# Performance work log

Measured on AMD Instinct MI355X. Metric: run time of the kernel, lower is better.

The kernel has to match this reference:

```python
import jax, jax.numpy as jnp
import numpy as np

LOG2PI = float(np.log(2.0 * np.pi))
BN_EPS = 1e-5


def _spn_layer(x, scopes, mean, std, sum_w, bn_w, bn_b):
    """Vectorized SPNLayer of SPNNeurons.
    x:      [B, F]
    scopes: [O, F] int, per-neuron permutation of feature indices
    mean/std: [O, F//2, n_mv, 2] gaussian leaf params (pairs of features)
    sum_w:  [O, F//2, n_mv] sum-node mixture weights (softmax-normalized)
    bn_w, bn_b: [O] batchnorm affine params (training-mode batch stats)
    returns [B, O]
    """
    B = x.shape[0]
    O, P, M, _ = mean.shape
    # gather permuted features and group into pairs: [B, O, P, 2]
    xp = x[:, scopes].reshape(B, O, P, 2)
    # gaussian leaf log-likelihoods: [B, O, P, M, 2]
    z = (xp[:, :, :, None, :] - mean) / std
    ll = -0.5 * (z * z) - jnp.log(std) - 0.5 * LOG2PI
    # product node over each pair: [B, O, P, M]
    prod = ll.sum(axis=-1)
    # sum node: weighted mixture in log domain: [B, O, P]
    logw = jax.nn.log_softmax(sum_w, axis=-1)
    s = jax.nn.logsumexp(prod + logw, axis=-1)
    # root product node over all pairs: [B, O]
    out = s.sum(axis=-1)
    # BatchNorm1d (training mode, biased variance)
    mu = out.mean(axis=0)
    var = ((out - mu) ** 2).mean(axis=0)
    return (out - mu) / jnp.sqrt(var + BN_EPS) * bn_w + bn_b


def setup_inputs() -> dict:
    key = jax.random.key(0)
    ks = jax.random.split(key, 12)
    B, F_IN = 32768, 784
    H1, O1, O2, OUT = 32, 16, 10, 10
    n_mv = 2

    rng = np.random.RandomState(0)
    scopes1 = jnp.asarray(np.stack([rng.permutation(H1) for _ in range(O1)]), dtype=jnp.int32)
    scopes2 = jnp.asarray(np.stack([rng.permutation(O1) for _ in range(O2)]), dtype=jnp.int32)

    x = jax.random.normal(ks[0], (B, F_IN), jnp.float32)
    W1 = jax.random.normal(ks[1], (H1, F_IN), jnp.float32) * np.sqrt(2.0 / F_IN)
    b1 = jnp.zeros((H1,), jnp.float32)

    mean1 = jax.random.normal(ks[2], (O1, H1 // 2, n_mv, 2), jnp.float32)
    std1 = jax.random.uniform(ks[3], (O1, H1 // 2, n_mv, 2), jnp.float32, 0.5, 1.5)
    sw1 = jax.random.uniform(ks[4], (O1, H1 // 2, n_mv), jnp.float32)
    bn1_w = jnp.ones((O1,), jnp.float32)
    bn1_b = jnp.zeros((O1,), jnp.float32)

    mean2 = jax.random.normal(ks[5], (O2, O1 // 2, n_mv, 2), jnp.float32)
    std2 = jax.random.uniform(ks[6], (O2, O1 // 2, n_mv, 2), jnp.float32, 0.5, 1.5)
    sw2 = jax.random.uniform(ks[7], (O2, O1 // 2, n_mv), jnp.float32)
    bn2_w = jnp.ones((O2,), jnp.float32)
    bn2_b = jnp.zeros((O2,), jnp.float32)

    W2 = jax.random.normal(ks[8], (OUT, O2), jnp.float32) * np.sqrt(2.0 / O2)
    b2 = jnp.zeros((OUT,), jnp.float32)

    return {"x": x, "W1": W1, "b1": b1,
            "mean1": mean1, "std1": std1, "sw1": sw1, "bn1_w": bn1_w, "bn1_b": bn1_b,
            "mean2": mean2, "std2": std2, "sw2": sw2, "bn2_w": bn2_w, "bn2_b": bn2_b,
            "W2": W2, "b2": b2, "scopes1": scopes1, "scopes2": scopes2}


def reference(x, W1, b1, mean1, std1, sw1, bn1_w, bn1_b,
              mean2, std2, sw2, bn2_w, bn2_b, W2, b2, scopes1, scopes2):
    h = jax.nn.relu(x @ W1.T + b1)                                  # [B, 32]
    h = _spn_layer(h, scopes1, mean1, std1, sw1, bn1_w, bn1_b)      # [B, 16]
    h = _spn_layer(h, scopes2, mean2, std2, sw2, bn2_w, bn2_b)      # [B, 10]
    logits = h @ W2.T + b2                                          # [B, 10]
    return jax.nn.log_softmax(logits, axis=1)
```

## Files before the change

### kernel.cpp

```cpp
#include <hip/hip_runtime.h>
#include <hip/hip_bf16.h>
#include <math.h>

#define LOG2PI_F 1.8378770664093453f
#define BN_EPS 1e-5f
#define BATCH 32768

#define K1_ROWS 64
#define NB1 (BATCH / K1_ROWS)
#define WS1 840
#define NB3 1024
#define RPB3 32

typedef __attribute__((ext_vector_type(8))) short bf16x8;
typedef __attribute__((ext_vector_type(4))) float f32x4;

__global__ __launch_bounds__(256) void k0_cvt(
    const float* __restrict__ W1, __hip_bfloat16* __restrict__ w1h,
    __hip_bfloat16* __restrict__ w1l)
{
    int i = blockIdx.x * 256 + threadIdx.x;
    if (i >= 32 * WS1) return;
    int o = i / WS1, k = i - o * WS1;
    float w = (k < 784) ? W1[o * 784 + k] : 0.f;
    __hip_bfloat16 h = __float2bfloat16(w);
    float hf = __bfloat162float(h);
    __hip_bfloat16 l = __float2bfloat16(w - hf);
    w1h[i] = h;
    w1l[i] = l;
}

__global__ __launch_bounds__(256, 2) void k1_gemm_spn1(
    const float* __restrict__ x,
    const __hip_bfloat16* __restrict__ w1h, const __hip_bfloat16* __restrict__ w1l,
    const float* __restrict__ b1,
    const float* __restrict__ mean1, const float* __restrict__ std1, const float* __restrict__ sw1,
    const int* __restrict__ scopes1,
    float* __restrict__ s1, float* __restrict__ partials1)
{
    __shared__ __hip_bfloat16 Ah[64][72];
    __shared__ __hip_bfloat16 Al[64][72];
    __shared__ float h_lds[64][33];
    __shared__ float mu_l[1024], inv_l[1024], c0_l[512];
    __shared__ int   sc_l[512];
    __shared__ float b1_l[32];
    __shared__ float sv_l[16][66];

    const int t = threadIdx.x;

    for (int il = t; il < 1024; il += 256) {
        int o = il & 15, rest = il >> 4;
        int f = rest & 1, m = (rest >> 1) & 1, p = rest >> 2;
        int ig = ((o * 16 + p) * 2 + m) * 2 + f;
        mu_l[il]  = mean1[ig];
        inv_l[il] = 1.0f / std1[ig];
    }
    for (int il = t; il < 512; il += 256) {
        int o = il & 15, rest = il >> 4;
        int m = rest & 1, p = rest >> 1;
        int igw = (o * 16 + p) * 2;
        float w0 = sw1[igw], w1v = sw1[igw + 1];
        float mx = fmaxf(w0, w1v);
        float lse = mx + __logf(__expf(w0 - mx) + __expf(w1v - mx));
        float wm = (m == 0) ? w0 : w1v;
        int igs = ((o * 16 + p) * 2 + m) * 2;
        c0_l[il] = (wm - lse) - __logf(std1[igs]) - __logf(std1[igs + 1]) - LOG2PI_F;
    }
    for (int il = t; il < 512; il += 256) sc_l[il] = scopes1[il];
    if (t < 32) b1_l[t] = b1[t];

    const int wid  = t >> 6;
    const int lane = t & 63;
    const int row0 = blockIdx.x * K1_ROWS;

    f32x4 acc0 = {0.f, 0.f, 0.f, 0.f};
    f32x4 acc1 = {0.f, 0.f, 0.f, 0.f};

    float4 xr[4];
    #pragma unroll
    for (int i = 0; i < 4; ++i) {
        int idx = i * 256 + t;
        int rr = idx >> 4, kq = idx & 15;
        xr[i] = *(const float4*)(x + (size_t)(row0 + rr) * 784 + kq * 4);
    }

    for (int c = 0; c < 13; ++c) {
        __syncthreads();
        #pragma unroll
        for (int i = 0; i < 4; ++i) {
            int idx = i * 256 + t;
            int rr = idx >> 4, kq = idx & 15;
            float4 v = xr[i];
            float vv[4] = {v.x, v.y, v.z, v.w};
            #pragma unroll
            for (int e = 0; e < 4; ++e) {
                __hip_bfloat16 h = __float2bfloat16(vv[e]);
                float hf = __bfloat162float(h);
                Ah[rr][kq * 4 + e] = h;
                Al[rr][kq * 4 + e] = __float2bfloat16(vv[e] - hf);
            }
        }
        __syncthreads();
        if (c < 12) {
            int kbase = (c + 1) * 64;
            #pragma unroll
            for (int i = 0; i < 4; ++i) {
                int idx = i * 256 + t;
                int rr = idx >> 4, kq = idx & 15;
                int kg = kbase + kq * 4;
                if (kg < 784)
                    xr[i] = *(const float4*)(x + (size_t)(row0 + rr) * 784 + kg);
                else
                    xr[i] = make_float4(0.f, 0.f, 0.f, 0.f);
            }
        }
        int nsteps = (c == 12) ? 1 : 2;
        for (int s = 0; s < nsteps; ++s) {
            int kloc = s * 32 + ((lane >> 4) & 3) * 8;
            int arow = wid * 16 + (lane & 15);
            bf16x8 ah = *(const bf16x8*)(&Ah[arow][kloc]);
            bf16x8 al = *(const bf16x8*)(&Al[arow][kloc]);
            int kb = c * 64 + kloc;
            int o0 = lane & 15;
            bf16x8 wh0 = *(const bf16x8*)(&w1h[o0 * WS1 + kb]);
            bf16x8 wl0 = *(const bf16x8*)(&w1l[o0 * WS1 + kb]);
            bf16x8 wh1 = *(const bf16x8*)(&w1h[(16 + o0) * WS1 + kb]);
            bf16x8 wl1 = *(const bf16x8*)(&w1l[(16 + o0) * WS1 + kb]);
            acc0 = __builtin_amdgcn_mfma_f32_16x16x32_bf16(ah, wh0, acc0, 0, 0, 0);
            acc0 = __builtin_amdgcn_mfma_f32_16x16x32_bf16(al, wh0, acc0, 0, 0, 0);
            acc0 = __builtin_amdgcn_mfma_f32_16x16x32_bf16(ah, wl0, acc0, 0, 0, 0);
            acc1 = __builtin_amdgcn_mfma_f32_16x16x32_bf16(ah, wh1, acc1, 0, 0, 0);
            acc1 = __builtin_amdgcn_mfma_f32_16x16x32_bf16(al, wh1, acc1, 0, 0, 0);
            acc1 = __builtin_amdgcn_mfma_f32_16x16x32_bf16(ah, wl1, acc1, 0, 0, 0);
        }
    }

    {
        int col = lane & 15;
        int rbase = wid * 16 + ((lane >> 4) & 3) * 4;
        #pragma unroll
        for (int r = 0; r < 4; ++r) {
            h_lds[rbase + r][col]      = fmaxf(acc0[r] + b1_l[col], 0.f);
            h_lds[rbase + r][16 + col] = fmaxf(acc1[r] + b1_l[16 + col], 0.f);
        }
    }
    __syncthreads();

    for (int task = t; task < 1024; task += 256) {
        int row_l = task >> 4, o = task & 15;
        float outv = 0.f;
        for (int p = 0; p < 16; ++p) {
            int f0 = sc_l[o * 32 + 2 * p], f1 = sc_l[o * 32 + 2 * p + 1];
            float x0 = h_lds[row_l][f0];
            float x1 = h_lds[row_l][f1];
            float vm[2];
            #pragma unroll
            for (int m = 0; m < 2; ++m) {
                int base = ((p * 2 + m) * 2) * 16 + o;
                float d0 = (x0 - mu_l[base])      * inv_l[base];
                float d1 = (x1 - mu_l[base + 16]) * inv_l[base + 16];
                vm[m] = c0_l[(p * 2 + m) * 16 + o] - 0.5f * (d0 * d0 + d1 * d1);
            }
            float a  = fmaxf(vm[0], vm[1]);
            float bm = fminf(vm[0], vm[1]);
            outv += a + __logf(1.f + __expf(bm - a));
        }
        s1[(size_t)(row0 + row_l) * 16 + o] = outv;
        sv_l[o][row_l] = outv;
    }
    __syncthreads();

    if (t < 16) {
        float s = 0.f;
        for (int rr = 0; rr < K1_ROWS; ++rr) s += sv_l[t][rr];
        float mb = s * (1.f / K1_ROWS);
        float m2 = 0.f;
        for (int rr = 0; rr < K1_ROWS; ++rr) { float d = sv_l[t][rr] - mb; m2 += d * d; }
        partials1[blockIdx.x * 32 + t]      = s;
        partials1[blockIdx.x * 32 + 16 + t] = m2;
    }
}

template <int NO, int NBLK, int RPB>
__global__ __launch_bounds__(256) void kreduce(
    const float* __restrict__ partials,
    const float* __restrict__ bn_w, const float* __restrict__ bn_b,
    float* __restrict__ stats)
{
    __shared__ double dsum[256];
    __shared__ double dmean[16];
    const int t = threadIdx.x;
    const int o = t & 15, seg = t >> 4;
    const int per = NBLK / 16;

    double s = 0.0;
    if (o < NO)
        for (int b = seg * per; b < (seg + 1) * per; ++b)
            s += (double)partials[b * (2 * NO) + o];
    dsum[t] = s;
    __syncthreads();
    if (t < 16) {
        double S = 0.0;
        for (int g = 0; g < 16; ++g) S += dsum[g * 16 + t];
        dmean[t] = S / (double)BATCH;
    }
    __syncthreads();
    double mean = dmean[o];
    double m2 = 0.0;
    if (o < NO) {
        for (int b = seg * per; b < (seg + 1) * per; ++b) {
            double bm = (double)partials[b * (2 * NO) + o] / (double)RPB;
            double d  = bm - mean;
            m2 += (double)partials[b * (2 * NO) + NO + o] + (double)RPB * d * d;
        }
    }
    __syncthreads();
    dsum[t] = m2;
    __syncthreads();
    if (t < NO) {
        double M2 = 0.0;
        for (int g = 0; g < 16; ++g) M2 += dsum[g * 16 + t];
        double var = M2 / (double)BATCH;
        double gsc = (double)bn_w[t] / sqrt(var + (double)BN_EPS);
        stats[t]      = (float)gsc;
        stats[NO + t] = (float)((double)bn_b[t] - dmean[t] * gsc);
    }
}

__global__ __launch_bounds__(320, 4) void k3_spn2(
    const float* __restrict__ s1,
    const float* __restrict__ mean2, const float* __restrict__ std2, const float* __restrict__ sw2,
    const int* __restrict__ scopes2, const float* __restrict__ stats1,
    float* __restrict__ s2, float* __restrict__ partials2)
{
    __shared__ float mu_l[320], inv_l[320], c0_l[160];
    __shared__ int   sc_l[160];
    __shared__ float sv_l[10 * 33];
    __shared__ float g_l[16], sh_l[16];

    const int t = threadIdx.x;

    if (t < 320) {
        int o = t % 10, rest = t / 10;
        int f = rest & 1, m = (rest >> 1) & 1, p = rest >> 2;
        int ig = ((o * 8 + p) * 2 + m) * 2 + f;
        mu_l[t]  = mean2[ig];
        inv_l[t] = 1.0f / std2[ig];
    }
    if (t < 160) {
        int o = t % 10, rest = t / 10;
        int m = rest & 1, p = rest >> 1;
        int igw = (o * 8 + p) * 2;
        float w0 = sw2[igw], w1 = sw2[igw + 1];
        float mx = fmaxf(w0, w1);
        float lse = mx + __logf(__expf(w0 - mx) + __expf(w1 - mx));
        float wm = (m == 0) ? w0 : w1;
        int igs = ((o * 8 + p) * 2 + m) * 2;
        c0_l[t] = (wm - lse) - __logf(std2[igs]) - __logf(std2[igs + 1]) - LOG2PI_F;
    }
    if (t < 160) sc_l[t] = scopes2[t];
    if (t < 16)  g_l[t]  = stats1[t];
    else if (t < 32) sh_l[t - 16] = stats1[t];
    __syncthreads();

    const int row_l = t / 10, o = t % 10;
    const int row = blockIdx.x * RPB3 + row_l;
    const float* s1r = s1 + (size_t)row * 16;

    float v[16];
    #pragma unroll
    for (int f = 0; f < 16; ++f) v[f] = fmaf(s1r[f], g_l[f], sh_l[f]);

    float outv = 0.f;
    for (int p = 0; p < 8; ++p) {
        int f0 = sc_l[o * 16 + 2 * p], f1 = sc_l[o * 16 + 2 * p + 1];
        float x0 = v[f0], x1 = v[f1];
        float vm[2];
        #pragma unroll
        for (int m = 0; m < 2; ++m) {
            int base = ((p * 2 + m) * 2) * 10 + o;
            float d0 = (x0 - mu_l[base])      * inv_l[base];
            float d1 = (x1 - mu_l[base + 10]) * inv_l[base + 10];
            vm[m] = c0_l[(p * 2 + m) * 10 + o] - 0.5f * (d0 * d0 + d1 * d1);
        }
        float a  = fmaxf(vm[0], vm[1]);
        float bm = fminf(vm[0], vm[1]);
        outv += a + __logf(1.f + __expf(bm - a));
    }
    s2[(size_t)row * 10 + o] = outv;
    sv_l[o * 33 + row_l] = outv;
    __syncthreads();

    if (t < 10) {
        float s = 0.f;
        for (int rr = 0; rr < RPB3; ++rr) s += sv_l[t * 33 + rr];
        float mb = s * (1.f / RPB3);
        float m2 = 0.f;
        for (int rr = 0; rr < RPB3; ++rr) { float d = sv_l[t * 33 + rr] - mb; m2 += d * d; }
        partials2[blockIdx.x * 20 + t]      = s;
        partials2[blockIdx.x * 20 + 10 + t] = m2;
    }
}

__global__ __launch_bounds__(256) void k5_head(
    const float* __restrict__ s2, const float* __restrict__ stats2,
    const float* __restrict__ W2, const float* __restrict__ b2,
    float* __restrict__ out)
{
    const int row = blockIdx.x * 256 + threadIdx.x;
    const float* sr = s2 + (size_t)row * 10;
    float v[10], l[10];
    #pragma unroll
    for (int o = 0; o < 10; ++o) v[o] = fmaf(sr[o], stats2[o], stats2[10 + o]);
    float mx = -1e30f;
    #pragma unroll
    for (int c = 0; c < 10; ++c) {
        float a = b2[c];
        #pragma unroll
        for (int o = 0; o < 10; ++o) a = fmaf(W2[c * 10 + o], v[o], a);
        l[c] = a;
        mx = fmaxf(mx, a);
    }
    float sum = 0.f;
    #pragma unroll
    for (int c = 0; c < 10; ++c) sum += __expf(l[c] - mx);
    float ls = mx + __logf(sum);
    float* orow = out + (size_t)row * 10;
    #pragma unroll
    for (int c = 0; c < 10; ++c) orow[c] = l[c] - ls;
}

extern "C" void kernel_launch(void* const* d_in, const int* in_sizes, int n_in,
                              void* d_out, int out_size, void* d_ws, size_t ws_size,
                              hipStream_t stream) {
    const float* x      = (const float*)d_in[0];
    const float* W1     = (const float*)d_in[1];
    const float* b1     = (const float*)d_in[2];
    const float* mean1  = (const float*)d_in[3];
    const float* std1   = (const float*)d_in[4];
    const float* sw1    = (const float*)d_in[5];
    const float* bn1_w  = (const float*)d_in[6];
    const float* bn1_b  = (const float*)d_in[7];
    const float* mean2  = (const float*)d_in[8];
    const float* std2   = (const float*)d_in[9];
    const float* sw2    = (const float*)d_in[10];
    const float* bn2_w  = (const float*)d_in[11];
    const float* bn2_b  = (const float*)d_in[12];
    const float* W2     = (const float*)d_in[13];
    const float* b2     = (const float*)d_in[14];
    const int*   sc1    = (const int*)d_in[15];
    const int*   sc2    = (const int*)d_in[16];
    float* out = (float*)d_out;

    __hip_bfloat16* w1h = (__hip_bfloat16*)d_ws;
    __hip_bfloat16* w1l = w1h + 32 * WS1;
    float* fbase = (float*)(w1l + 32 * WS1);
    float* s1  = fbase;
    float* s2  = s1 + 32768 * 16;
    float* p1  = s2 + 32768 * 10;
    float* p2  = p1 + NB1 * 32;
    float* st1 = p2 + NB3 * 20;
    float* st2 = st1 + 32;

    hipLaunchKernelGGL(k0_cvt, dim3((32 * WS1 + 255) / 256), dim3(256), 0, stream,
                       W1, w1h, w1l);
    hipLaunchKernelGGL(k1_gemm_spn1, dim3(NB1), dim3(256), 0, stream,
                       x, w1h, w1l, b1, mean1, std1, sw1, sc1, s1, p1);
    hipLaunchKernelGGL((kreduce<16, NB1, K1_ROWS>), dim3(1), dim3(256), 0, stream, p1, bn1_w, bn1_b, st1);
    hipLaunchKernelGGL(k3_spn2, dim3(NB3), dim3(320), 0, stream,
                       s1, mean2, std2, sw2, sc2, st1, s2, p2);
    hipLaunchKernelGGL((kreduce<10, NB3, RPB3>), dim3(1), dim3(256), 0, stream, p2, bn2_w, bn2_b, st2);
    hipLaunchKernelGGL(k5_head, dim3(32768 / 256), dim3(256), 0, stream,
                       s2, st2, W2, b2, out);
}
```

Baseline: 236.4 us.

## Load GEMM operands straight to registers with software-pipelined prefetch, drop LDS staging

```diff
diff --git a/kernel.cpp b/kernel.cpp
--- a/kernel.cpp
+++ b/kernel.cpp
@@ -14,6 +14,15 @@
 
 typedef __attribute__((ext_vector_type(8))) short bf16x8;
 typedef __attribute__((ext_vector_type(4))) float f32x4;
+
+__device__ __forceinline__ short f2bf_s(float f) {
+    union { __hip_bfloat16 b; short s; } u;
+    u.b = __float2bfloat16(f);
+    return u.s;
+}
+__device__ __forceinline__ float bfs_to_f(short s) {
+    return __uint_as_float(((unsigned)(unsigned short)s) << 16);
+}
 
 __global__ __launch_bounds__(256) void k0_cvt(
     const float* __restrict__ W1, __hip_bfloat16* __restrict__ w1h,
@@ -30,6 +39,44 @@
     w1l[i] = l;
 }
 
+struct Step { float4 a0, a1; bf16x8 wh0, wl0, wh1, wl1; };
+
+__device__ __forceinline__ void load_step(
+    Step& S, const float* __restrict__ xrow,
+    const __hip_bfloat16* __restrict__ wh, const __hip_bfloat16* __restrict__ wl,
+    int s, int kgrp, int o0)
+{
+    int kb = s * 32 + kgrp * 8;
+    int kc = (kb < 784) ? kb : 0;
+    S.a0 = *(const float4*)(xrow + kc);
+    S.a1 = *(const float4*)(xrow + kc + 4);
+    const __hip_bfloat16* ph = wh + o0 * WS1 + kb;
+    const __hip_bfloat16* pl = wl + o0 * WS1 + kb;
+    S.wh0 = *(const bf16x8*)(ph);
+    S.wh1 = *(const bf16x8*)(ph + 16 * WS1);
+    S.wl0 = *(const bf16x8*)(pl);
+    S.wl1 = *(const bf16x8*)(pl + 16 * WS1);
+}
+
+__device__ __forceinline__ void comp_step(const Step& S, f32x4& acc0, f32x4& acc1)
+{
+    float av[8] = {S.a0.x, S.a0.y, S.a0.z, S.a0.w, S.a1.x, S.a1.y, S.a1.z, S.a1.w};
+    bf16x8 ah, al;
+    #pragma unroll
+    for (int e = 0; e < 8; ++e) {
+        float f = av[e];
+        short h = f2bf_s(f);
+        ah[e] = h;
+        al[e] = f2bf_s(f - bfs_to_f(h));
+    }
+    acc0 = __builtin_amdgcn_mfma_f32_16x16x32_bf16(ah, S.wh0, acc0, 0, 0, 0);
+    acc0 = __builtin_amdgcn_mfma_f32_16x16x32_bf16(al, S.wh0, acc0, 0, 0, 0);
+    acc0 = __builtin_amdgcn_mfma_f32_16x16x32_bf16(ah, S.wl0, acc0, 0, 0, 0);
+    acc1 = __builtin_amdgcn_mfma_f32_16x16x32_bf16(ah, S.wh1, acc1, 0, 0, 0);
+    acc1 = __builtin_amdgcn_mfma_f32_16x16x32_bf16(al, S.wh1, acc1, 0, 0, 0);
+    acc1 = __builtin_amdgcn_mfma_f32_16x16x32_bf16(ah, S.wl1, acc1, 0, 0, 0);
+}
+
 __global__ __launch_bounds__(256, 2) void k1_gemm_spn1(
     const float* __restrict__ x,
     const __hip_bfloat16* __restrict__ w1h, const __hip_bfloat16* __restrict__ w1l,
@@ -38,8 +85,6 @@
     const int* __restrict__ scopes1,
     float* __restrict__ s1, float* __restrict__ partials1)
 {
-    __shared__ __hip_bfloat16 Ah[64][72];
-    __shared__ __hip_bfloat16 Al[64][72];
     __shared__ float h_lds[64][33];
     __shared__ float mu_l[1024], inv_l[1024], c0_l[512];
     __shared__ int   sc_l[512];
@@ -72,68 +117,42 @@
     const int wid  = t >> 6;
     const int lane = t & 63;
     const int row0 = blockIdx.x * K1_ROWS;
+    const int kgrp = (lane >> 4) & 3;
+    const int o0   = lane & 15;
+    const float* xrow = x + (size_t)(row0 + wid * 16 + (lane & 15)) * 784;
 
     f32x4 acc0 = {0.f, 0.f, 0.f, 0.f};
     f32x4 acc1 = {0.f, 0.f, 0.f, 0.f};
 
-    float4 xr[4];
-    #pragma unroll
-    for (int i = 0; i < 4; ++i) {
-        int idx = i * 256 + t;
-        int rr = idx >> 4, kq = idx & 15;
-        xr[i] = *(const float4*)(x + (size_t)(row0 + rr) * 784 + kq * 4);
-    }
-
-    for (int c = 0; c < 13; ++c) {
-        __syncthreads();
-        #pragma unroll
-        for (int i = 0; i < 4; ++i) {
-            int idx = i * 256 + t;
-            int rr = idx >> 4, kq = idx & 15;
-            float4 v = xr[i];
-            float vv[4] = {v.x, v.y, v.z, v.w};
-            #pragma unroll
-            for (int e = 0; e < 4; ++e) {
-                __hip_bfloat16 h = __float2bfloat16(vv[e]);
-                float hf = __bfloat162float(h);
-                Ah[rr][kq * 4 + e] = h;
-                Al[rr][kq * 4 + e] = __float2bfloat16(vv[e] - hf);
-            }
+    Step A0, A1, A2, B0, B1, B2;
+    load_step(A0, xrow, w1h, w1l, 0, kgrp, o0);
+    load_step(A1, xrow, w1h, w1l, 1, kgrp, o0);
+    load_step(A2, xrow, w1h, w1l, 2, kgrp, o0);
+    #pragma unroll
+    for (int gg = 0; gg < 4; ++gg) {
+        int g0 = gg * 6;
+        load_step(B0, xrow, w1h, w1l, g0 + 3, kgrp, o0);
+        load_step(B1, xrow, w1h, w1l, g0 + 4, kgrp, o0);
+        load_step(B2, xrow, w1h, w1l, g0 + 5, kgrp, o0);
+        comp_step(A0, acc0, acc1);
+        comp_step(A1, acc0, acc1);
+        comp_step(A2, acc0, acc1);
+        if (gg < 3) {
+            load_step(A0, xrow, w1h, w1l, g0 + 6, kgrp, o0);
+            load_step(A1, xrow, w1h, w1l, g0 + 7, kgrp, o0);
+            load_step(A2, xrow, w1h, w1l, g0 + 8, kgrp, o0);
         }
-        __syncthreads();
-        if (c < 12) {
-            int kbase = (c + 1) * 64;
-            #pragma unroll
-            for (int i = 0; i < 4; ++i) {
-                int idx = i * 256 + t;
-                int rr = idx >> 4, kq = idx & 15;
-                int kg = kbase + kq * 4;
-                if (kg < 784)
-                    xr[i] = *(const float4*)(x + (size_t)(row0 + rr) * 784 + kg);
-                else
-                    xr[i] = make_float4(0.f, 0.f, 0.f, 0.f);
-            }
-        }
-        int nsteps = (c == 12) ? 1 : 2;
-        for (int s = 0; s < nsteps; ++s) {
-            int kloc = s * 32 + ((lane >> 4) & 3) * 8;
-            int arow = wid * 16 + (lane & 15);
-            bf16x8 ah = *(const bf16x8*)(&Ah[arow][kloc]);
-            bf16x8 al = *(const bf16x8*)(&Al[arow][kloc]);
-            int kb = c * 64 + kloc;
-            int o0 = lane & 15;
-            bf16x8 wh0 = *(const bf16x8*)(&w1h[o0 * WS1 + kb]);
-            bf16x8 wl0 = *(const bf16x8*)(&w1l[o0 * WS1 + kb]);
-            bf16x8 wh1 = *(const bf16x8*)(&w1h[(16 + o0) * WS1 + kb]);
-            bf16x8 wl1 = *(const bf16x8*)(&w1l[(16 + o0) * WS1 + kb]);
-            acc0 = __builtin_amdgcn_mfma_f32_16x16x32_bf16(ah, wh0, acc0, 0, 0, 0);
-            acc0 = __builtin_amdgcn_mfma_f32_16x16x32_bf16(al, wh0, acc0, 0, 0, 0);
-            acc0 = __builtin_amdgcn_mfma_f32_16x16x32_bf16(ah, wl0, acc0, 0, 0, 0);
-            acc1 = __builtin_amdgcn_mfma_f32_16x16x32_bf16(ah, wh1, acc1, 0, 0, 0);
-            acc1 = __builtin_amdgcn_mfma_f32_16x16x32_bf16(al, wh1, acc1, 0, 0, 0);
-            acc1 = __builtin_amdgcn_mfma_f32_16x16x32_bf16(ah, wl1, acc1, 0, 0, 0);
-        }
-    }
+        comp_step(B0, acc0, acc1);
+        comp_step(B1, acc0, acc1);
+        comp_step(B2, acc0, acc1);
+    }
+    {
+        Step T;
+        load_step(T, xrow, w1h, w1l, 24, kgrp, o0);
+        comp_step(T, acc0, acc1);
+    }
+
+    __syncthreads();
 
     {
         int col = lane & 15;
@@ -235,10 +254,12 @@
 {
     __shared__ float mu_l[320], inv_l[320], c0_l[160];
     __shared__ int   sc_l[160];
-    __shared__ float sv_l[10 * 33];
+    __shared__ float v_lds[32][17];
+    __shared__ float sv_l[10][33];
     __shared__ float g_l[16], sh_l[16];
 
     const int t = threadIdx.x;
+    const int row0 = blockIdx.x * RPB3;
 
     if (t < 320) {
         int o = t % 10, rest = t / 10;
@@ -260,21 +281,20 @@
     }
     if (t < 160) sc_l[t] = scopes2[t];
     if (t < 16)  g_l[t]  = stats1[t];
-    else if (t < 32) sh_l[t - 16] = stats1[t];
+    else if (t >= 64 && t < 80) sh_l[t - 64] = stats1[16 + (t - 64)];
+    __syncthreads();
+
+    for (int i = t; i < 512; i += 320) {
+        int rl = i >> 4, f = i & 15;
+        v_lds[rl][f] = fmaf(s1[(size_t)(row0 + rl) * 16 + f], g_l[f], sh_l[f]);
+    }
     __syncthreads();
 
     const int row_l = t / 10, o = t % 10;
-    const int row = blockIdx.x * RPB3 + row_l;
-    const float* s1r = s1 + (size_t)row * 16;
-
-    float v[16];
-    #pragma unroll
-    for (int f = 0; f < 16; ++f) v[f] = fmaf(s1r[f], g_l[f], sh_l[f]);
-
     float outv = 0.f;
     for (int p = 0; p < 8; ++p) {
         int f0 = sc_l[o * 16 + 2 * p], f1 = sc_l[o * 16 + 2 * p + 1];
-        float x0 = v[f0], x1 = v[f1];
+        float x0 = v_lds[row_l][f0], x1 = v_lds[row_l][f1];
         float vm[2];
         #pragma unroll
         for (int m = 0; m < 2; ++m) {
@@ -287,37 +307,48 @@
         float bm = fminf(vm[0], vm[1]);
         outv += a + __logf(1.f + __expf(bm - a));
     }
-    s2[(size_t)row * 10 + o] = outv;
-    sv_l[o * 33 + row_l] = outv;
+    s2[(size_t)(row0 + row_l) * 10 + o] = outv;
+    sv_l[o][row_l] = outv;
     __syncthreads();
 
     if (t < 10) {
         float s = 0.f;
-        for (int rr = 0; rr < RPB3; ++rr) s += sv_l[t * 33 + rr];
+        for (int rr = 0; rr < RPB3; ++rr) s += sv_l[t][rr];
         float mb = s * (1.f / RPB3);
         float m2 = 0.f;
-        for (int rr = 0; rr < RPB3; ++rr) { float d = sv_l[t * 33 + rr] - mb; m2 += d * d; }
+        for (int rr = 0; rr < RPB3; ++rr) { float d = sv_l[t][rr] - mb; m2 += d * d; }
         partials2[blockIdx.x * 20 + t]      = s;
         partials2[blockIdx.x * 20 + 10 + t] = m2;
     }
 }
 
-__global__ __launch_bounds__(256) void k5_head(
+__global__ __launch_bounds__(128) void k5_head(
     const float* __restrict__ s2, const float* __restrict__ stats2,
     const float* __restrict__ W2, const float* __restrict__ b2,
     float* __restrict__ out)
 {
-    const int row = blockIdx.x * 256 + threadIdx.x;
+    __shared__ float w2_l[100], b2_l[10], st_l[20];
+    const int t = threadIdx.x;
+    if (t < 100) w2_l[t] = W2[t];
+    if (t < 10)  b2_l[t] = b2[t];
+    if (t < 20)  st_l[t] = stats2[t];
+    __syncthreads();
+
+    const int row = blockIdx.x * 128 + t;
     const float* sr = s2 + (size_t)row * 10;
     float v[10], l[10];
     #pragma unroll
-    for (int o = 0; o < 10; ++o) v[o] = fmaf(sr[o], stats2[o], stats2[10 + o]);
+    for (int i = 0; i < 5; ++i) {
+        float2 p = *(const float2*)(sr + 2 * i);
+        v[2*i]   = fmaf(p.x, st_l[2*i],   st_l[10 + 2*i]);
+        v[2*i+1] = fmaf(p.y, st_l[2*i+1], st_l[10 + 2*i+1]);
+    }
     float mx = -1e30f;
     #pragma unroll
     for (int c = 0; c < 10; ++c) {
-        float a = b2[c];
+        float a = b2_l[c];
         #pragma unroll
-        for (int o = 0; o < 10; ++o) a = fmaf(W2[c * 10 + o], v[o], a);
+        for (int o = 0; o < 10; ++o) a = fmaf(w2_l[c * 10 + o], v[o], a);
         l[c] = a;
         mx = fmaxf(mx, a);
     }
@@ -370,6 +401,6 @@
     hipLaunchKernelGGL(k3_spn2, dim3(NB3), dim3(320), 0, stream,
                        s1, mean2, std2, sw2, sc2, st1, s2, p2);
     hipLaunchKernelGGL((kreduce<10, NB3, RPB3>), dim3(1), dim3(256), 0, stream, p2, bn2_w, bn2_b, st2);
-    hipLaunchKernelGGL(k5_head, dim3(32768 / 256), dim3(256), 0, stream,
+    hipLaunchKernelGGL(k5_head, dim3(BATCH / 128), dim3(128), 0, stream,
                        s2, st2, W2, b2, out);
 }
```

Measured after the change: 236.3 us. No clear change (-0.1%).
